# Kernel tuning notes

Measured on AMD Instinct MI355X. Metric: run time of the kernel, lower is better.

Reference implementation:

```python
import math
import jax, jax.numpy as jnp
import numpy as np

IMG = 512; P = 16; CIN = 3; COUT = 3; E = 768; NHEADS = 12; L = 8
NPH = IMG // P            # 32 patches per side
N = NPH * NPH             # 1024 tokens (must match learned 1024x1024 attn bias)
HD = E // NHEADS          # 64
INTER = min(E // 2, 128)  # 128, OutputProjection intermediate
EPS = 1e-5


def _sin_pe(n_h, n_w, d):
    # faithful port of get_2d_sinusoidal_encoding (second half stays zero)
    pe = np.zeros((n_h, n_w, d), dtype=np.float32)
    dq, dh = d // 4, d // 2
    div = np.exp(np.arange(0, dq, 2, dtype=np.float32) * (-math.log(10000.0) / dq))
    pr = np.arange(n_h, dtype=np.float32)[:, None]
    pc = np.arange(n_w, dtype=np.float32)[:, None]
    pe[:, :, 0:dq:2] = np.sin(pr * div)[:, None, :]
    pe[:, :, 1:dq:2] = np.cos(pr * div)[:, None, :]
    pe[:, :, dq:dh:2] = np.sin(pc * div)[None, :, :]
    pe[:, :, dq + 1:dh:2] = np.cos(pc * div)[None, :, :]
    return jnp.asarray(pe.reshape(-1, d))


def _ln(x, g, b):
    m = x.mean(-1, keepdims=True)
    v = ((x - m) ** 2).mean(-1, keepdims=True)
    return (x - m) * jax.lax.rsqrt(v + EPS) * g + b


def setup_inputs():
    key = jax.random.key(0)
    ks = iter(jax.random.split(key, 32))
    def nrm(shape, scale=0.02):
        return jax.random.normal(next(ks), shape, jnp.float32) * scale
    return {
        'x': jax.random.normal(next(ks), (2, CIN, IMG, IMG), jnp.float32),
        'conv_w': nrm((E, CIN, P, P)), 'conv_b': jnp.zeros((E,), jnp.float32),
        'ln1_g': jnp.ones((L, E), jnp.float32), 'ln1_b': jnp.zeros((L, E), jnp.float32),
        'qkv_w': nrm((L, 3 * E, E)),
        'proj_w': nrm((L, E, E)), 'proj_b': jnp.zeros((L, E), jnp.float32),
        'attn_bias': jax.random.normal(next(ks), (L, N, N), jnp.float32),  # torch.randn init
        'ln2_g': jnp.ones((L, E), jnp.float32), 'ln2_b': jnp.zeros((L, E), jnp.float32),
        'mlp_w1': nrm((L, 2 * E, E)), 'mlp_b1': jnp.zeros((L, 2 * E), jnp.float32),
        'mlp_w2': nrm((L, E, 2 * E)), 'mlp_b2': jnp.zeros((L, E), jnp.float32),
        'op_w1': nrm((INTER, E)), 'op_b1': jnp.zeros((INTER,), jnp.float32),
        'op_w2': nrm((P * P * COUT, INTER)), 'op_b2': jnp.zeros((P * P * COUT,), jnp.float32),
        'ag_wg': nrm((1, COUT), 0.2), 'ag_bng_w': jnp.ones((), jnp.float32), 'ag_bng_b': jnp.zeros((), jnp.float32),
        'ag_wx': nrm((1, CIN), 0.2), 'ag_bnx_w': jnp.ones((), jnp.float32), 'ag_bnx_b': jnp.zeros((), jnp.float32),
        'ag_psi_w': jnp.full((), 0.5, jnp.float32), 'ag_psi_b': jnp.zeros((), jnp.float32),
    }


def reference(x, conv_w, conv_b, ln1_g, ln1_b, qkv_w, proj_w, proj_b, attn_bias,
              ln2_g, ln2_b, mlp_w1, mlp_b1, mlp_w2, mlp_b2,
              op_w1, op_b1, op_w2, op_b2,
              ag_wg, ag_bng_w, ag_bng_b, ag_wx, ag_bnx_w, ag_bnx_b, ag_psi_w, ag_psi_b):
    B = x.shape[0]
    # --- VisionTransformerInput: patch-embed conv (stride == kernel) as reshape+GEMM ---
    xp = x.reshape(B, CIN, NPH, P, NPH, P).transpose(0, 2, 4, 1, 3, 5).reshape(B, N, CIN * P * P)
    t = xp @ conv_w.reshape(E, -1).T + conv_b
    t = t + _sin_pe(NPH, NPH, E)[None]

    # --- encoder blocks (scan over stacked per-layer params) ---
    def block(t, p):
        y = _ln(t, p['ln1_g'], p['ln1_b'])
        qkv = (y @ p['qkv_w'].T).reshape(B, N, 3, NHEADS, HD).transpose(2, 0, 3, 1, 4)
        q, k, v = qkv[0], qkv[1], qkv[2]
        s = jnp.einsum('bhnd,bhmd->bhnm', q, k) / math.sqrt(HD)
        # NOTE: relative_position_bias is computed but never added in the source (dead code);
        # only the learned (N,N) bias parameter is added.
        s = s + p['attn_bias'][None, None]
        a = jax.nn.softmax(s, axis=-1)
        o = jnp.einsum('bhnm,bhmd->bhnd', a, v).transpose(0, 2, 1, 3).reshape(B, N, E)
        o = o @ p['proj_w'].T + p['proj_b']
        t = t + (y + o)  # MHA has an extra internal residual (out = x + out) in the source
        h = _ln(t, p['ln2_g'], p['ln2_b'])
        h = jax.nn.gelu(h @ p['mlp_w1'].T + p['mlp_b1'], approximate=False) @ p['mlp_w2'].T + p['mlp_b2']
        return t + h, None

    stacked = {'ln1_g': ln1_g, 'ln1_b': ln1_b, 'qkv_w': qkv_w, 'proj_w': proj_w,
               'proj_b': proj_b, 'attn_bias': attn_bias, 'ln2_g': ln2_g, 'ln2_b': ln2_b,
               'mlp_w1': mlp_w1, 'mlp_b1': mlp_b1, 'mlp_w2': mlp_w2, 'mlp_b2': mlp_b2}
    t, _ = jax.lax.scan(block, t, stacked)

    # --- OutputProjection: MLP -> Fold -> attention gate -> (identity) interpolate ---
    h = jax.nn.relu(t @ op_w1.T + op_b1) @ op_w2.T + op_b2  # (B, N, C*P*P)
    # nn.Fold(kernel=stride=P): columns interpreted as (C, P, P)
    g = h.reshape(B, NPH, NPH, COUT, P, P).transpose(0, 3, 1, 4, 2, 5).reshape(B, COUT, IMG, IMG)
    inv = 1.0 / math.sqrt(1.0 + EPS)  # BatchNorm eval: running_mean=0, running_var=1
    g1 = jnp.einsum('bchw,oc->bohw', g, ag_wg) * (inv * ag_bng_w) + ag_bng_b
    x1 = jnp.einsum('bchw,oc->bohw', x, ag_wx) * (inv * ag_bnx_w) + ag_bnx_b
    psi = jax.nn.sigmoid(jax.nn.relu(g1 + x1) * ag_psi_w + ag_psi_b)
    out = g * (x * psi)  # x * att_gate's psi == skip_gated; then x_fold * skip_gated
    # F.interpolate to (output_size, output_size) with output_size == image_size: identity
    return out
```

## Files before the change

kernel.cpp:

```cpp
#include <hip/hip_runtime.h>
#include <math.h>

typedef unsigned short u16;
typedef unsigned int u32;
typedef __attribute__((ext_vector_type(8))) short bf16x8;
typedef __attribute__((ext_vector_type(16))) float f32x16;
typedef __attribute__((ext_vector_type(4))) float f4v;
typedef __attribute__((ext_vector_type(4))) u32 u32x4;

#define MFMA(a, b, c) __builtin_amdgcn_mfma_f32_32x32x16_bf16(a, b, c, 0, 0, 0)

#define SYNC_STEP() do {                                   \
    asm volatile("s_waitcnt vmcnt(0)" ::: "memory");       \
    __builtin_amdgcn_s_barrier();                          \
    __builtin_amdgcn_sched_barrier(0);                     \
} while (0)

#define SYNC_CNT6() do {                                   \
    asm volatile("s_waitcnt vmcnt(6)" ::: "memory");       \
    __builtin_amdgcn_s_barrier();                          \
    __builtin_amdgcn_sched_barrier(0);                     \
} while (0)

__device__ __forceinline__ float bf2f(u16 h) { return __uint_as_float(((u32)h) << 16); }

__device__ __forceinline__ void split2(float v, u16& h, u16& l) {
    u32 u = __float_as_uint(v);
    u32 hr = (u + 0x7FFFu + ((u >> 16) & 1u)) & 0xFFFF0000u;
    h = (u16)(hr >> 16);
    float lf = v - __uint_as_float(hr);
    u32 ul = __float_as_uint(lf);
    l = (u16)((ul + 0x7FFFu + ((ul >> 16) & 1u)) >> 16);
}

__device__ __forceinline__ u32 cvtpk(float lo, float hi) {
    u32 r;
    asm("v_cvt_pk_bf16_f32 %0, %1, %2" : "=v"(r) : "v"(lo), "v"(hi));
    return r;
}

__device__ __forceinline__ void swap32(u32& a, u32& b, int hi) {
    u32 ta = (u32)__shfl_xor((int)a, 32);
    u32 tb = (u32)__shfl_xor((int)b, 32);
    u32 na = hi ? tb : a;
    u32 nb = hi ? b : ta;
    a = na; b = nb;
}

__device__ __forceinline__ void repack(const f32x16& v, int base, int hi, bf16x8& fh, bf16x8& fl) {
    float p0 = v[base + 0], p1 = v[base + 1], p2 = v[base + 2], p3 = v[base + 3];
    float p4 = v[base + 4], p5 = v[base + 5], p6 = v[base + 6], p7 = v[base + 7];
    u32 X0 = cvtpk(p0, p1), X1 = cvtpk(p2, p3), X4 = cvtpk(p4, p5), X5 = cvtpk(p6, p7);
    float r0 = p0 - __uint_as_float(X0 << 16);
    float r1 = p1 - __uint_as_float(X0 & 0xFFFF0000u);
    float r2 = p2 - __uint_as_float(X1 << 16);
    float r3 = p3 - __uint_as_float(X1 & 0xFFFF0000u);
    float r4 = p4 - __uint_as_float(X4 << 16);
    float r5 = p5 - __uint_as_float(X4 & 0xFFFF0000u);
    float r6 = p6 - __uint_as_float(X5 << 16);
    float r7 = p7 - __uint_as_float(X5 & 0xFFFF0000u);
    u32 L0 = cvtpk(r0, r1), L1 = cvtpk(r2, r3), L4 = cvtpk(r4, r5), L5 = cvtpk(r6, r7);
    swap32(X0, X4, hi); swap32(X1, X5, hi);
    swap32(L0, L4, hi); swap32(L1, L5, hi);
    u32x4 th = {X0, X1, X4, X5};
    u32x4 tl = {L0, L1, L4, L5};
    fh = __builtin_bit_cast(bf16x8, th);
    fl = __builtin_bit_cast(bf16x8, tl);
}

__global__ __launch_bounds__(256) void pe_kernel(float* __restrict__ pe) {
    int idx = blockIdx.x * 256 + threadIdx.x;
    int n = idx / 768, d = idx - n * 768;
    float v = 0.0f;
    if (d < 384) {
        int pos = (d < 192) ? (n >> 5) : (n & 31);
        int dd  = (d < 192) ? d : d - 192;
        int j2  = dd & ~1;
        float dv  = expf((float)j2 * (-9.210340371976184f / 192.0f));
        float ang = (float)pos * dv;
        v = (dd & 1) ? cosf(ang) : sinf(ang);
    }
    pe[idx] = v;
}

__global__ __launch_bounds__(256) void gather_kernel(const float* __restrict__ x,
                                                     u16* __restrict__ xph,
                                                     u16* __restrict__ xpl) {
    int idx = blockIdx.x * 256 + threadIdx.x;
    int m = idx / 768, col = idx - m * 768;
    int b = m >> 10, n = m & 1023;
    int ci = col >> 8, rem = col & 255;
    int pr = rem >> 4, pc = rem & 15;
    int hh = ((n >> 5) << 4) + pr;
    int ww = ((n & 31) << 4) + pc;
    float v = x[(((size_t)(b * 3 + ci) * 512) + hh) * 512 + ww];
    split2(v, xph[idx], xpl[idx]);
}

__global__ __launch_bounds__(256) void fsplit(const float* __restrict__ in,
                                              u16* __restrict__ h, u16* __restrict__ l, int n4) {
    int i = blockIdx.x * 256 + threadIdx.x;
    if (i >= n4) return;
    float4 v = ((const float4*)in)[i];
    int o = i * 4;
    split2(v.x, h[o], l[o]);
    split2(v.y, h[o + 1], l[o + 1]);
    split2(v.z, h[o + 2], l[o + 2]);
    split2(v.w, h[o + 3], l[o + 3]);
}

__global__ __launch_bounds__(256) void wsplit_layer(const float* __restrict__ qkvw,
                                                    const float* __restrict__ projw,
                                                    const float* __restrict__ w1,
                                                    const float* __restrict__ w2,
                                                    u16* __restrict__ wh, u16* __restrict__ wl) {
    int i4 = blockIdx.x * 256 + threadIdx.x;
    if (i4 >= 1179648) return;
    size_t idx = (size_t)i4 * 4;
    const float* src; size_t off;
    if (idx < 1769472)      { src = qkvw;  off = idx; }
    else if (idx < 2359296) { src = projw; off = idx - 1769472; }
    else if (idx < 3538944) { src = w1;    off = idx - 2359296; }
    else                    { src = w2;    off = idx - 3538944; }
    float4 v = *(const float4*)(src + off);
    split2(v.x, wh[idx], wl[idx]);
    split2(v.y, wh[idx + 1], wl[idx + 1]);
    split2(v.z, wh[idx + 2], wl[idx + 2]);
    split2(v.w, wh[idx + 3], wl[idx + 3]);
}

__global__ __launch_bounds__(256) void btrans(const float* __restrict__ src, float* __restrict__ dst) {
    __shared__ float tl[32][33];
    int bx = blockIdx.x & 31, by = blockIdx.x >> 5;
    int tx = threadIdx.x & 31, ty = threadIdx.x >> 5;
#pragma unroll
    for (int j = 0; j < 4; ++j)
        tl[ty + j * 8][tx] = src[(size_t)(by * 32 + ty + j * 8) * 1024 + bx * 32 + tx];
    __syncthreads();
#pragma unroll
    for (int j = 0; j < 4; ++j)
        dst[(size_t)(bx * 32 + ty + j * 8) * 1024 + by * 32 + tx] = tl[tx][ty + j * 8];
}

__global__ __launch_bounds__(256) void ln_kernel(const float* __restrict__ x,
                                                 const float* __restrict__ g,
                                                 const float* __restrict__ b,
                                                 u16* __restrict__ yh, u16* __restrict__ yl) {
    int row = blockIdx.x, tid = threadIdx.x;
    const float* xr = x + (size_t)row * 768;
    float v0 = xr[tid], v1 = xr[tid + 256], v2 = xr[tid + 512];
    __shared__ float red[256];
    red[tid] = v0 + v1 + v2;
    __syncthreads();
    for (int off = 128; off > 0; off >>= 1) {
        if (tid < off) red[tid] += red[tid + off];
        __syncthreads();
    }
    float mean = red[0] * (1.0f / 768.0f);
    __syncthreads();
    float d0 = v0 - mean, d1 = v1 - mean, d2 = v2 - mean;
    red[tid] = d0 * d0 + d1 * d1 + d2 * d2;
    __syncthreads();
    for (int off = 128; off > 0; off >>= 1) {
        if (tid < off) red[tid] += red[tid + off];
        __syncthreads();
    }
    float rstd = rsqrtf(red[0] * (1.0f / 768.0f) + 1e-5f);
    size_t o = (size_t)row * 768;
    split2(d0 * rstd * g[tid]       + b[tid],       yh[o + tid],       yl[o + tid]);
    split2(d1 * rstd * g[tid + 256] + b[tid + 256], yh[o + tid + 256], yl[o + tid + 256]);
    split2(d2 * rstd * g[tid + 512] + b[tid + 512], yh[o + tid + 512], yl[o + tid + 512]);
}

__device__ __forceinline__ int mrow(int r) { return (r + (r >> 2)) & 3; }

template <int MODE>
__global__ __launch_bounds__(256, 2) void gemm_sp(const u16* __restrict__ Ah, const u16* __restrict__ Al,
                                                  const u16* __restrict__ Bh, const u16* __restrict__ Bl,
                                                  const float* __restrict__ bias,
                                                  const float* __restrict__ res,
                                                  const float* __restrict__ auxf,
                                                  const u16* __restrict__ auxh, const u16* __restrict__ auxl,
                                                  float* __restrict__ C, u16* __restrict__ Ch, u16* __restrict__ Cl,
                                                  u16* __restrict__ Cth, u16* __restrict__ Ctl,
                                                  int M, int N, int K, int nby) {
    __shared__ u16 SH[36864];
    u16* As = SH;
    u16* Bs = SH + 12288;
    int tid = threadIdx.x;
    int wid = tid >> 6, lane = tid & 63;
    int hi = lane >> 5;
    int lq = lane & 31;
    int wm = wid >> 1, wn = wid & 1;

    int nwg = gridDim.x;
    int q8 = nwg >> 3;
    int swz = (blockIdx.x & 7) * q8 + (blockIdx.x >> 3);
    int cb = swz / nby, rb = swz - cb * nby;
    int m0 = rb * 64, n0 = cb * 128;

    f32x16 acc0 = {}, acc1 = {};

    auto stage = [&](int buf, int kt) {
#pragma unroll
        for (int c = 0; c < 2; ++c) {
            const u16* G = c ? Al : Ah;
            int row = wid * 16 + (lane >> 2);
            int ch = (lane & 3) ^ mrow(row);
            const u16* g = G + (size_t)(m0 + row) * K + kt + ch * 8;
            __builtin_amdgcn_global_load_lds((const __attribute__((address_space(1))) u32*)g,
                                             (__attribute__((address_space(3))) u32*)&As[(buf * 2 + c) * 2048 + (wid * 16) * 32],
                                             16, 0, 0);
        }
#pragma unroll
        for (int c = 0; c < 2; ++c) {
            const u16* G = c ? Bl : Bh;
#pragma unroll
            for (int j = 0; j < 2; ++j) {
                int row = wid * 32 + j * 16 + (lane >> 2);
                int ch = (lane & 3) ^ mrow(row);
                const u16* g = G + (size_t)(n0 + row) * K + kt + ch * 8;
                __builtin_amdgcn_global_load_lds((const __attribute__((address_space(1))) u32*)g,
                                                 (__attribute__((address_space(3))) u32*)&Bs[(buf * 2 + c) * 4096 + (wid * 32 + j * 16) * 32],
                                                 16, 0, 0);
            }
        }
    };

    int ar  = wm * 32 + lq;
    int br0 = wn * 64 + lq;
    int br1 = br0 + 32;

    auto compute = [&](int buf) {
#pragma unroll
        for (int kc = 0; kc < 2; ++kc) {
            int gc = (kc << 1) | hi;
            int oA  = ar  * 32 + ((gc ^ mrow(ar))  << 3);
            int oB0 = br0 * 32 + ((gc ^ mrow(br0)) << 3);
            int oB1 = br1 * 32 + ((gc ^ mrow(br1)) << 3);
            bf16x8 ah  = *(const bf16x8*)(As + (buf * 2 + 0) * 2048 + oA);
            bf16x8 al  = *(const bf16x8*)(As + (buf * 2 + 1) * 2048 + oA);
            bf16x8 b0h = *(const bf16x8*)(Bs + (buf * 2 + 0) * 4096 + oB0);
            bf16x8 b0l = *(const bf16x8*)(Bs + (buf * 2 + 1) * 4096 + oB0);
            bf16x8 b1h = *(const bf16x8*)(Bs + (buf * 2 + 0) * 4096 + oB1);
            bf16x8 b1l = *(const bf16x8*)(Bs + (buf * 2 + 1) * 4096 + oB1);
            acc0 = MFMA(ah, b0h, acc0);
            acc0 = MFMA(ah, b0l, acc0);
            acc0 = MFMA(al, b0h, acc0);
            acc1 = MFMA(ah, b1h, acc1);
            acc1 = MFMA(ah, b1l, acc1);
            acc1 = MFMA(al, b1h, acc1);
        }
    };

    int nk = K >> 5;
    stage(0, 0);
    stage(1, 32);
    int t = 0;
    for (; t < nk - 1; ++t) {
        SYNC_CNT6();
        if (t + 2 < nk) stage((t + 2) % 3, (t + 2) << 5);
        compute(t % 3);
    }
    SYNC_STEP();
    compute(t % 3);

    if (MODE == 7 && n0 >= 1536) {
        __syncthreads();
        auto scatterV = [&](const f32x16& a, int fn) {
            int c = wn * 64 + fn * 32 + lq;
            int rb2 = wm * 32 + (hi << 2);
#pragma unroll
            for (int r = 0; r < 16; ++r) {
                int rr = rb2 + (r & 3) + ((r >> 2) << 3);
                u16 hv, lv;
                split2(a[r], hv, lv);
                SH[c * 68 + rr] = hv;
                SH[8704 + c * 68 + rr] = lv;
            }
        };
        scatterV(acc0, 0);
        scatterV(acc1, 1);
        __syncthreads();
        int bb = m0 >> 10;
        int nbase = m0 & 1023;
#pragma unroll
        for (int pass = 0; pass < 4; ++pass) {
            int c2 = pass * 32 + (tid >> 3);
            int ch8 = tid & 7;
            int hcol = (n0 - 1536) + c2;
            int h2 = hcol >> 6, hd = hcol & 63;
            size_t dst = ((size_t)(bb * 12 + h2) * 64 + hd) * 1024 + nbase + ch8 * 8;
            int so = c2 * 68 + ch8 * 8;
            u32x4 ph = {*(const u32*)&SH[so], *(const u32*)&SH[so + 2],
                        *(const u32*)&SH[so + 4], *(const u32*)&SH[so + 6]};
            u32x4 pl = {*(const u32*)&SH[8704 + so], *(const u32*)&SH[8704 + so + 2],
                        *(const u32*)&SH[8704 + so + 4], *(const u32*)&SH[8704 + so + 6]};
            *(u32x4*)(Cth + dst) = ph;
            *(u32x4*)(Ctl + dst) = pl;
        }
        return;
    }

    auto epi = [&](const f32x16& a, int fn) {
        int col = n0 + wn * 64 + fn * 32 + lq;
        int rb2 = m0 + wm * 32 + (hi << 2);
#pragma unroll
        for (int r = 0; r < 16; ++r) {
            int row = rb2 + (r & 3) + ((r >> 2) << 3);
            float v = a[r];
            size_t o = (size_t)row * N + col;
            if (MODE == 1) C[o] = v + bias[col] + auxf[(size_t)(row & 1023) * N + col];
            else if (MODE == 2) C[o] = res[o] + (bf2f(auxh[o]) + bf2f(auxl[o])) + v + bias[col];
            else if (MODE == 3) {
                v += bias[col];
                v = 0.5f * v * (1.0f + erff(v * 0.70710678118654752f));
                split2(v, Ch[o], Cl[o]);
            }
            else if (MODE == 4) C[o] = res[o] + v + bias[col];
            else if (MODE == 5) {
                v += bias[col];
                v = fmaxf(v, 0.0f);
                split2(v, Ch[o], Cl[o]);
            }
            else if (MODE == 6) C[o] = v + bias[col];
            else if (MODE == 7) {
                size_t o7 = (size_t)row * 1536 + col;
                split2(v, Ch[o7], Cl[o7]);
            }
        }
    };
    epi(acc0, 0); epi(acc1, 1);
}

__global__ __launch_bounds__(256, 2) void attn_mfma(const u16* __restrict__ qh, const u16* __restrict__ ql,
                                                    const u16* __restrict__ vth, const u16* __restrict__ vtl,
                                                    const float* __restrict__ biasT,
                                                    u16* __restrict__ oh, u16* __restrict__ ol) {
    __shared__ u16 smem[2][2][4][2048];
    int tid = threadIdx.x;
    int wid = tid >> 6, lane = tid & 63;
    int s = wid & 1, p = wid >> 1;
    int lq = lane & 31;
    int hi = lane >> 5;
    int id = blockIdx.x;
    int xcd = id & 7;
    int j = id >> 3;
    int bh = xcd * 3 + (j >> 4);
    int qt = j & 15;
    int b = bh / 12, h = bh % 12;
    int bq0 = qt * 64;
    int gq = bq0 + s * 32 + lq;

    bf16x8 qfh[4], qfl[4];
    {
        size_t qo = (size_t)(b * 1024 + gq) * 1536 + h * 64 + hi * 8;
#pragma unroll
        for (int ks = 0; ks < 4; ++ks) {
            qfh[ks] = *(const bf16x8*)(qh + qo + ks * 16);
            qfl[ks] = *(const bf16x8*)(ql + qo + ks * 16);
        }
    }

    f32x16 oa = {}, ob = {};
    float m_i = -1e30f, l_i = 0.0f;

    auto stage = [&](int buf, int kb) {
        if (s == 0) {
#pragma unroll
            for (int c = 0; c < 2; ++c) {
                const u16* G = c ? ql : qh;
#pragma unroll
                for (int i = 0; i < 4; ++i) {
                    int r = 8 * i + (lane >> 3);
                    int cl = (lane & 7) ^ (r & 7);
                    const u16* g = G + (size_t)(b * 1024 + kb + r) * 1536 + 768 + h * 64 + cl * 8;
                    __builtin_amdgcn_global_load_lds((const __attribute__((address_space(1))) u32*)g,
                                                     (__attribute__((address_space(3))) u32*)&smem[p][buf][c][i * 512],
                                                     16, 0, 0);
                }
            }
        } else {
#pragma unroll
            for (int c = 0; c < 2; ++c) {
                const u16* G = c ? vtl : vth;
#pragma unroll
                for (int i = 0; i < 4; ++i) {
                    int r = 16 * i + (lane >> 2);
                    int cl = (lane & 3) ^ ((r >> 1) & 3);
                    const u16* g = G + ((size_t)(b * 12 + h) * 64 + r) * 1024 + kb + cl * 8;
                    __builtin_amdgcn_global_load_lds((const __attribute__((address_space(1))) u32*)g,
                                                     (__attribute__((address_space(3))) u32*)&smem[p][buf][2 + c][i * 512],
                                                     16, 0, 0);
                }
            }
        }
    };

    auto compute = [&](int buf, int kb) {
        const u16* Kh = &smem[p][buf][0][0];
        const u16* Kl = &smem[p][buf][1][0];
        const u16* Vh = &smem[p][buf][2][0];
        const u16* Vl = &smem[p][buf][3][0];
        const float* bbase = biasT + (size_t)(kb + 4 * hi) * 1024 + gq;
        float bb[16];
#pragma unroll
        for (int g2 = 0; g2 < 4; ++g2)
#pragma unroll
            for (int q = 0; q < 4; ++q)
                bb[g2 * 4 + q] = bbase[(size_t)(g2 * 8 + q) * 1024];
        f32x16 sa = {};
#pragma unroll
        for (int ks = 0; ks < 4; ++ks) {
            int off = lq * 64 + (((2 * ks + hi) ^ (lq & 7)) << 3);
            bf16x8 kha = *(const bf16x8*)(Kh + off);
            bf16x8 kla = *(const bf16x8*)(Kl + off);
            sa = MFMA(kha, qfh[ks], sa);
            sa = MFMA(kha, qfl[ks], sa);
            sa = MFMA(kla, qfh[ks], sa);
        }
        bf16x8 vf[2][4];
#pragma unroll
        for (int kslot = 0; kslot < 2; ++kslot) {
            int offa = lq * 32 + (((2 * kslot + hi) ^ ((lq >> 1) & 3)) << 3);
            vf[kslot][0] = *(const bf16x8*)(Vh + offa);
            vf[kslot][1] = *(const bf16x8*)(Vh + offa + 1024);
            vf[kslot][2] = *(const bf16x8*)(Vl + offa);
            vf[kslot][3] = *(const bf16x8*)(Vl + offa + 1024);
        }
#pragma unroll
        for (int r = 0; r < 16; ++r) sa[r] = sa[r] * 0.125f + bb[r];
        float mt = sa[0];
#pragma unroll
        for (int r = 1; r < 16; ++r) mt = fmaxf(mt, sa[r]);
        mt = fmaxf(mt, __shfl_xor(mt, 32));
        float mnew = fmaxf(m_i, mt);
        int up = __any(mnew > m_i);
        float scl = __expf(m_i - mnew);
        m_i = mnew;
        float ls = 0.0f;
#pragma unroll
        for (int r = 0; r < 16; ++r) { sa[r] = __expf(sa[r] - mnew); ls += sa[r]; }
        ls += __shfl_xor(ls, 32);
        l_i = l_i * scl + ls;
        if (up) {
#pragma unroll
            for (int r = 0; r < 16; ++r) {
                int qr = (r & 3) + 8 * (r >> 2) + 4 * hi;
                float fr = __shfl(scl, qr);
                oa[r] *= fr; ob[r] *= fr;
            }
        }
#pragma unroll
        for (int kslot = 0; kslot < 2; ++kslot) {
            bf16x8 ph, pl;
            repack(sa, kslot * 8, hi, ph, pl);
            oa = MFMA(ph, vf[kslot][0], oa);
            oa = MFMA(ph, vf[kslot][2], oa);
            oa = MFMA(pl, vf[kslot][0], oa);
            ob = MFMA(ph, vf[kslot][1], ob);
            ob = MFMA(ph, vf[kslot][3], ob);
            ob = MFMA(pl, vf[kslot][1], ob);
        }
    };

    stage(0, p * 32);
    for (int ss = 0; ss < 16; ss += 2) {
        SYNC_STEP();
        if (ss + 1 < 16) stage(1, (2 * (ss + 1) + p) * 32);
        compute(0, (2 * ss + p) * 32);
        SYNC_STEP();
        if (ss + 2 < 16) stage(0, (2 * (ss + 2) + p) * 32);
        compute(1, (2 * (ss + 1) + p) * 32);
    }
    __syncthreads();

    float* mlb = (float*)((char*)smem + 32768);
    mlb[((s * 2 + p) * 2 + 0) * 32 + lq] = m_i;
    mlb[((s * 2 + p) * 2 + 1) * 32 + lq] = l_i;
    __syncthreads();
    float mo  = mlb[((s * 2 + (p ^ 1)) * 2 + 0) * 32 + lq];
    float lo_ = mlb[((s * 2 + (p ^ 1)) * 2 + 1) * 32 + lq];
    float M = fmaxf(m_i, mo);
    float ea = __expf(m_i - M), eb = __expf(mo - M);
    float L = ea * l_i + eb * lo_;
    float f = ea / L;
    float frv[16];
#pragma unroll
    for (int r = 0; r < 16; ++r) frv[r] = __shfl(f, (r & 3) + 8 * (r >> 2) + 4 * hi);
    float* ox = (float*)((char*)smem + s * 8192);
    if (p == 1) {
#pragma unroll
        for (int r = 0; r < 16; ++r) {
            int qr = (r & 3) + 8 * (r >> 2) + 4 * hi;
            ox[qr * 64 + lq] = oa[r] * frv[r];
            ox[qr * 64 + 32 + lq] = ob[r] * frv[r];
        }
    }
    __syncthreads();
    if (p == 0) {
#pragma unroll
        for (int r = 0; r < 16; ++r) {
            int qr = (r & 3) + 8 * (r >> 2) + 4 * hi;
            float va = oa[r] * frv[r] + ox[qr * 64 + lq];
            float vb = ob[r] * frv[r] + ox[qr * 64 + 32 + lq];
            size_t d = (size_t)(b * 1024 + bq0 + s * 32 + qr) * 768 + h * 64;
            split2(va, oh[d + lq], ol[d + lq]);
            split2(vb, oh[d + 32 + lq], ol[d + 32 + lq]);
        }
    }
}

__global__ __launch_bounds__(256) void fold_gate(const float* __restrict__ hbuf,
                                                 const float* __restrict__ xin,
                                                 const float* __restrict__ wg,
                                                 const float* __restrict__ bngw,
                                                 const float* __restrict__ bngb,
                                                 const float* __restrict__ wx,
                                                 const float* __restrict__ bnxw,
                                                 const float* __restrict__ bnxb,
                                                 const float* __restrict__ psiw,
                                                 const float* __restrict__ psib,
                                                 float* __restrict__ out) {
    int idx = blockIdx.x * 256 + threadIdx.x;
    int b = idx >> 18;
    int rem = idx & 262143;
    int hh = rem >> 9, ww = rem & 511;
    int n = ((hh >> 4) << 5) + (ww >> 4);
    int pr = hh & 15, pc = ww & 15;
    const float* hrow = hbuf + (size_t)(b * 1024 + n) * 768 + pr * 16 + pc;
    float g0 = hrow[0], g1 = hrow[256], g2 = hrow[512];
    size_t xoff = ((size_t)(b * 3) * 512 + hh) * 512 + ww;
    float x0 = xin[xoff], x1 = xin[xoff + 262144], x2 = xin[xoff + 524288];
    float inv = rsqrtf(1.0f + 1e-5f);
    float gg = (g0 * wg[0] + g1 * wg[1] + g2 * wg[2]) * inv * bngw[0] + bngb[0];
    float xx = (x0 * wx[0] + x1 * wx[1] + x2 * wx[2]) * inv * bnxw[0] + bnxb[0];
    float z = gg + xx;
    z = z > 0.0f ? z : 0.0f;
    float psi = 1.0f / (1.0f + expf(-(z * psiw[0] + psib[0])));
    out[xoff]          = g0 * x0 * psi;
    out[xoff + 262144] = g1 * x1 * psi;
    out[xoff + 524288] = g2 * x2 * psi;
}

extern "C" void kernel_launch(void* const* d_in, const int* in_sizes, int n_in,
                              void* d_out, int out_size, void* d_ws, size_t ws_size,
                              hipStream_t stream) {
    (void)in_sizes; (void)n_in; (void)out_size; (void)ws_size;
    const float* x       = (const float*)d_in[0];
    const float* conv_w  = (const float*)d_in[1];
    const float* conv_b  = (const float*)d_in[2];
    const float* ln1_g   = (const float*)d_in[3];
    const float* ln1_b   = (const float*)d_in[4];
    const float* qkv_w   = (const float*)d_in[5];
    const float* proj_w  = (const float*)d_in[6];
    const float* proj_b  = (const float*)d_in[7];
    const float* attn_bs = (const float*)d_in[8];
    const float* ln2_g   = (const float*)d_in[9];
    const float* ln2_b   = (const float*)d_in[10];
    const float* mlp_w1  = (const float*)d_in[11];
    const float* mlp_b1  = (const float*)d_in[12];
    const float* mlp_w2  = (const float*)d_in[13];
    const float* mlp_b2  = (const float*)d_in[14];
    const float* op_w1   = (const float*)d_in[15];
    const float* op_b1   = (const float*)d_in[16];
    const float* op_w2   = (const float*)d_in[17];
    const float* op_b2   = (const float*)d_in[18];
    const float* ag_wg   = (const float*)d_in[19];
    const float* ag_bngw = (const float*)d_in[20];
    const float* ag_bngb = (const float*)d_in[21];
    const float* ag_wx   = (const float*)d_in[22];
    const float* ag_bnxw = (const float*)d_in[23];
    const float* ag_bnxb = (const float*)d_in[24];
    const float* ag_psiw = (const float*)d_in[25];
    const float* ag_psib = (const float*)d_in[26];
    float* out = (float*)d_out;

    char* w8 = (char*)d_ws;
    float* t     = (float*)(w8);
    u16* yh      = (u16*)(w8 + 6291456);
    u16* yl      = (u16*)(w8 + 9437184);
    u16* ath     = (u16*)(w8 + 12582912);
    u16* atl     = (u16*)(w8 + 15728640);
    u16* mh      = (u16*)(w8 + 18874368);
    u16* ml      = (u16*)(w8 + 25165824);
    u16* qh      = (u16*)(w8 + 31457280);
    u16* ql      = (u16*)(w8 + 37748736);
    u16* wh      = (u16*)(w8 + 44040192);
    u16* wl      = (u16*)(w8 + 53477376);
    float* biasT = (float*)(w8 + 62914560);
    float* pe  = (float*)qh;
    u16* xph = mh; u16* xpl = ml;
    u16* vth = mh; u16* vtl = ml;
    float* oph2 = (float*)qh;
    u16* o1h = ath; u16* o1l = atl;

    const size_t W_QKV = 0, W_PROJ = 1769472, W_MLP1 = 2359296, W_MLP2 = 3538944;

    pe_kernel<<<3072, 256, 0, stream>>>(pe);
    gather_kernel<<<6144, 256, 0, stream>>>(x, xph, xpl);
    fsplit<<<576, 256, 0, stream>>>(conv_w, wh, wl, 147456);
    gemm_sp<1><<<192, 256, 0, stream>>>(xph, xpl, wh, wl, conv_b, nullptr, pe,
                                        nullptr, nullptr, t, nullptr, nullptr,
                                        nullptr, nullptr, 2048, 768, 768, 32);

    for (int l = 0; l < 8; ++l) {
        wsplit_layer<<<4608, 256, 0, stream>>>(qkv_w + (size_t)l * 1769472, proj_w + (size_t)l * 589824,
                                               mlp_w1 + (size_t)l * 1179648, mlp_w2 + (size_t)l * 1179648,
                                               wh, wl);
        btrans<<<1024, 256, 0, stream>>>(attn_bs + (size_t)l * 1048576, biasT);
        ln_kernel<<<2048, 256, 0, stream>>>(t, ln1_g + l * 768, ln1_b + l * 768, yh, yl);
        gemm_sp<7><<<576, 256, 0, stream>>>(yh, yl, wh + W_QKV, wl + W_QKV, nullptr, nullptr,
                                            nullptr, nullptr, nullptr, nullptr, qh, ql,
                                            vth, vtl, 2048, 2304, 768, 32);
        attn_mfma<<<384, 256, 0, stream>>>(qh, ql, vth, vtl, biasT, ath, atl);
        gemm_sp<2><<<192, 256, 0, stream>>>(ath, atl, wh + W_PROJ, wl + W_PROJ, proj_b + l * 768,
                                            t, nullptr, yh, yl, t, nullptr, nullptr,
                                            nullptr, nullptr, 2048, 768, 768, 32);
        ln_kernel<<<2048, 256, 0, stream>>>(t, ln2_g + l * 768, ln2_b + l * 768, yh, yl);
        gemm_sp<3><<<384, 256, 0, stream>>>(yh, yl, wh + W_MLP1, wl + W_MLP1, mlp_b1 + l * 1536,
                                            nullptr, nullptr, nullptr, nullptr, nullptr, mh, ml,
                                            nullptr, nullptr, 2048, 1536, 768, 32);
        gemm_sp<4><<<192, 256, 0, stream>>>(mh, ml, wh + W_MLP2, wl + W_MLP2, mlp_b2 + l * 768,
                                            t, nullptr, nullptr, nullptr, t, nullptr, nullptr,
                                            nullptr, nullptr, 2048, 768, 1536, 32);
    }

    fsplit<<<1536, 256, 0, stream>>>(t, yh, yl, 393216);
    fsplit<<<96, 256, 0, stream>>>(op_w1, wh, wl, 24576);
    fsplit<<<96, 256, 0, stream>>>(op_w2, wh + 131072, wl + 131072, 24576);
    gemm_sp<5><<<32, 256, 0, stream>>>(yh, yl, wh, wl, op_b1, nullptr, nullptr,
                                       nullptr, nullptr, nullptr, o1h, o1l,
                                       nullptr, nullptr, 2048, 128, 768, 32);
    gemm_sp<6><<<192, 256, 0, stream>>>(o1h, o1l, wh + 131072, wl + 131072, op_b2, nullptr,
                                        nullptr, nullptr, nullptr, oph2, nullptr, nullptr,
                                        nullptr, nullptr, 2048, 768, 128, 32);
    fold_gate<<<2048, 256, 0, stream>>>(oph2, x, ag_wg, ag_bngw, ag_bngb,
                                        ag_wx, ag_bnxw, ag_bnxb, ag_psiw, ag_psib, out);
}
```

Measured before the change: 1.463 ms.

## Prefetch attention bias, split QK accumulators, lazy softmax rescale, shuffle LayerNorm

The attention inner loop now loads the next tile's bias one step ahead, alongside the K/V staging, so the load latency is hidden behind the current compute. QK^T is split into two independent MFMA accumulator chains to shorten dependency stalls. s_setprio is raised around the MFMA blocks. Online softmax now rescales only when the max grows by more than 8, and the max reduction uses a tree. LayerNorm replaces its shared-memory tree reduction with wave shuffles, trading extra registers for fewer barriers.

```diff
diff --git a/kernel.cpp b/kernel.cpp
--- a/kernel.cpp
+++ b/kernel.cpp
@@ -147,25 +147,23 @@
                                                  const float* __restrict__ b,
                                                  u16* __restrict__ yh, u16* __restrict__ yl) {
     int row = blockIdx.x, tid = threadIdx.x;
+    int wid = tid >> 6, lane = tid & 63;
     const float* xr = x + (size_t)row * 768;
     float v0 = xr[tid], v1 = xr[tid + 256], v2 = xr[tid + 512];
-    __shared__ float red[256];
-    red[tid] = v0 + v1 + v2;
+    __shared__ float ws[8];
+    float sum = v0 + v1 + v2;
+#pragma unroll
+    for (int off = 32; off > 0; off >>= 1) sum += __shfl_xor(sum, off);
+    if (lane == 0) ws[wid] = sum;
     __syncthreads();
-    for (int off = 128; off > 0; off >>= 1) {
-        if (tid < off) red[tid] += red[tid + off];
-        __syncthreads();
-    }
-    float mean = red[0] * (1.0f / 768.0f);
+    float mean = (ws[0] + ws[1] + ws[2] + ws[3]) * (1.0f / 768.0f);
+    float d0 = v0 - mean, d1 = v1 - mean, d2 = v2 - mean;
+    float vs = d0 * d0 + d1 * d1 + d2 * d2;
+#pragma unroll
+    for (int off = 32; off > 0; off >>= 1) vs += __shfl_xor(vs, off);
+    if (lane == 0) ws[4 + wid] = vs;
     __syncthreads();
-    float d0 = v0 - mean, d1 = v1 - mean, d2 = v2 - mean;
-    red[tid] = d0 * d0 + d1 * d1 + d2 * d2;
-    __syncthreads();
-    for (int off = 128; off > 0; off >>= 1) {
-        if (tid < off) red[tid] += red[tid + off];
-        __syncthreads();
-    }
-    float rstd = rsqrtf(red[0] * (1.0f / 768.0f) + 1e-5f);
+    float rstd = rsqrtf((ws[4] + ws[5] + ws[6] + ws[7]) * (1.0f / 768.0f) + 1e-5f);
     size_t o = (size_t)row * 768;
     split2(d0 * rstd * g[tid]       + b[tid],       yh[o + tid],       yl[o + tid]);
     split2(d1 * rstd * g[tid + 256] + b[tid + 256], yh[o + tid + 256], yl[o + tid + 256]);
@@ -397,28 +395,38 @@
         }
     };
 
-    auto compute = [&](int buf, int kb) {
+    auto loadBias = [&](float (&bb)[16], int kb) {
+        const float* bbase = biasT + (size_t)(kb + 4 * hi) * 1024 + gq;
+#pragma unroll
+        for (int g2 = 0; g2 < 4; ++g2)
+#pragma unroll
+            for (int q = 0; q < 4; ++q)
+                bb[g2 * 4 + q] = bbase[(size_t)(g2 * 8 + q) * 1024];
+    };
+
+    auto compute = [&](int buf, const float (&bb)[16]) {
         const u16* Kh = &smem[p][buf][0][0];
         const u16* Kl = &smem[p][buf][1][0];
         const u16* Vh = &smem[p][buf][2][0];
         const u16* Vl = &smem[p][buf][3][0];
-        const float* bbase = biasT + (size_t)(kb + 4 * hi) * 1024 + gq;
-        float bb[16];
-#pragma unroll
-        for (int g2 = 0; g2 < 4; ++g2)
-#pragma unroll
-            for (int q = 0; q < 4; ++q)
-                bb[g2 * 4 + q] = bbase[(size_t)(g2 * 8 + q) * 1024];
-        f32x16 sa = {};
-#pragma unroll
-        for (int ks = 0; ks < 4; ++ks) {
-            int off = lq * 64 + (((2 * ks + hi) ^ (lq & 7)) << 3);
-            bf16x8 kha = *(const bf16x8*)(Kh + off);
-            bf16x8 kla = *(const bf16x8*)(Kl + off);
-            sa = MFMA(kha, qfh[ks], sa);
-            sa = MFMA(kha, qfl[ks], sa);
-            sa = MFMA(kla, qfh[ks], sa);
-        }
+        f32x16 s0 = {}, s1 = {};
+        __builtin_amdgcn_s_setprio(1);
+#pragma unroll
+        for (int ks = 0; ks < 2; ++ks) {
+            int offA = lq * 64 + (((2 * ks + hi) ^ (lq & 7)) << 3);
+            int offB = lq * 64 + (((2 * (ks + 2) + hi) ^ (lq & 7)) << 3);
+            bf16x8 khA = *(const bf16x8*)(Kh + offA);
+            bf16x8 klA = *(const bf16x8*)(Kl + offA);
+            bf16x8 khB = *(const bf16x8*)(Kh + offB);
+            bf16x8 klB = *(const bf16x8*)(Kl + offB);
+            s0 = MFMA(khA, qfh[ks], s0);
+            s1 = MFMA(khB, qfh[ks + 2], s1);
+            s0 = MFMA(khA, qfl[ks], s0);
+            s1 = MFMA(khB, qfl[ks + 2], s1);
+            s0 = MFMA(klA, qfh[ks], s0);
+            s1 = MFMA(klB, qfh[ks + 2], s1);
+        }
+        __builtin_amdgcn_s_setprio(0);
         bf16x8 vf[2][4];
 #pragma unroll
         for (int kslot = 0; kslot < 2; ++kslot) {
@@ -428,22 +436,21 @@
             vf[kslot][2] = *(const bf16x8*)(Vl + offa);
             vf[kslot][3] = *(const bf16x8*)(Vl + offa + 1024);
         }
-#pragma unroll
-        for (int r = 0; r < 16; ++r) sa[r] = sa[r] * 0.125f + bb[r];
-        float mt = sa[0];
-#pragma unroll
-        for (int r = 1; r < 16; ++r) mt = fmaxf(mt, sa[r]);
-        mt = fmaxf(mt, __shfl_xor(mt, 32));
-        float mnew = fmaxf(m_i, mt);
-        int up = __any(mnew > m_i);
-        float scl = __expf(m_i - mnew);
-        m_i = mnew;
-        float ls = 0.0f;
-#pragma unroll
-        for (int r = 0; r < 16; ++r) { sa[r] = __expf(sa[r] - mnew); ls += sa[r]; }
-        ls += __shfl_xor(ls, 32);
-        l_i = l_i * scl + ls;
-        if (up) {
+        f32x16 sa;
+#pragma unroll
+        for (int r = 0; r < 16; ++r) sa[r] = (s0[r] + s1[r]) * 0.125f + bb[r];
+        float m01 = fmaxf(sa[0], sa[1]),  m23 = fmaxf(sa[2], sa[3]);
+        float m45 = fmaxf(sa[4], sa[5]),  m67 = fmaxf(sa[6], sa[7]);
+        float m89 = fmaxf(sa[8], sa[9]),  mab = fmaxf(sa[10], sa[11]);
+        float mcd = fmaxf(sa[12], sa[13]), mef = fmaxf(sa[14], sa[15]);
+        float pm = fmaxf(fmaxf(fmaxf(m01, m23), fmaxf(m45, m67)),
+                         fmaxf(fmaxf(m89, mab), fmaxf(mcd, mef)));
+        pm = fmaxf(pm, __shfl_xor(pm, 32));
+        if (__any(pm > m_i + 8.0f)) {
+            float mnew = fmaxf(m_i, pm);
+            float scl = __expf(m_i - mnew);
+            m_i = mnew;
+            l_i *= scl;
 #pragma unroll
             for (int r = 0; r < 16; ++r) {
                 int qr = (r & 3) + 8 * (r >> 2) + 4 * hi;
@@ -451,6 +458,12 @@
                 oa[r] *= fr; ob[r] *= fr;
             }
         }
+        float ls = 0.0f;
+#pragma unroll
+        for (int r = 0; r < 16; ++r) { sa[r] = __expf(sa[r] - m_i); ls += sa[r]; }
+        ls += __shfl_xor(ls, 32);
+        l_i += ls;
+        __builtin_amdgcn_s_setprio(1);
 #pragma unroll
         for (int kslot = 0; kslot < 2; ++kslot) {
             bf16x8 ph, pl;
@@ -462,16 +475,19 @@
             ob = MFMA(ph, vf[kslot][3], ob);
             ob = MFMA(pl, vf[kslot][1], ob);
         }
+        __builtin_amdgcn_s_setprio(0);
     };
 
+    float bbA[16], bbB[16];
     stage(0, p * 32);
+    loadBias(bbA, p * 32);
     for (int ss = 0; ss < 16; ss += 2) {
         SYNC_STEP();
-        if (ss + 1 < 16) stage(1, (2 * (ss + 1) + p) * 32);
-        compute(0, (2 * ss + p) * 32);
+        if (ss + 1 < 16) { stage(1, (2 * (ss + 1) + p) * 32); loadBias(bbB, (2 * (ss + 1) + p) * 32); }
+        compute(0, bbA);
         SYNC_STEP();
-        if (ss + 2 < 16) stage(0, (2 * (ss + 2) + p) * 32);
-        compute(1, (2 * (ss + 1) + p) * 32);
+        if (ss + 2 < 16) { stage(0, (2 * (ss + 2) + p) * 32); loadBias(bbA, (2 * (ss + 2) + p) * 32); }
+        compute(1, bbB);
     }
     __syncthreads();
 
```

Result: faster. 1.427 ms (-2.5%).
